# Kernel optimization log

Hardware: AMD Instinct MI355X
Metric: run time of the kernel (lower is better)

Reference implementation:

```python
import jax, jax.numpy as jnp
import numpy as np

N_NODES = 100000
N_EDGES = 1000000
D_IN = 64
D_HID = 64


def gcn_norm(edge_index, edge_weight, num_nodes):
    """PyG gcn_norm with add_self_loops=True, fill_value=1.0.
    Returns augmented (row, col, norm) including self loops."""
    loop = jnp.arange(num_nodes)
    row = jnp.concatenate([edge_index[0], loop])
    col = jnp.concatenate([edge_index[1], loop])
    ew = jnp.concatenate([edge_weight, jnp.ones((num_nodes,), edge_weight.dtype)])
    deg = jnp.zeros((num_nodes,), ew.dtype).at[col].add(ew)
    dinv = jnp.where(deg > 0, jax.lax.rsqrt(deg), 0.0).astype(ew.dtype)
    norm = dinv[row] * ew * dinv[col]  # [E + N]
    return row, col, norm


def gcn_conv(h, row, col, norm, W, b, num_nodes):
    """out[col] += norm * (h @ W)[row]; then add bias."""
    hw = h @ W  # [N, d_out] dense transform first (as PyG GCNConv)
    msg = norm[:, None] * hw[row]  # gather + scale  [E+N, d_out]
    out = jnp.zeros((num_nodes, W.shape[1]), h.dtype).at[col].add(msg)
    return out + b


def setup_inputs() -> dict:
    key = jax.random.key(0)
    ks = jax.random.split(key, 12)
    x = jax.random.normal(ks[0], (N_NODES, D_IN), jnp.float32)
    edge_index = jax.random.randint(ks[1], (2, N_EDGES), 0, N_NODES, jnp.int64)
    edge_weight = jax.random.uniform(ks[2], (N_EDGES,), jnp.float32)
    batch = jnp.zeros((N_NODES,), jnp.int64)

    def glorot(k, fan_in, fan_out):
        s = jnp.sqrt(6.0 / (fan_in + fan_out))
        return jax.random.uniform(k, (fan_in, fan_out), jnp.float32, -s, s)

    return {
        "x": x, "edge_index": edge_index, "edge_weight": edge_weight, "batch": batch,
        "W_in": glorot(ks[3], D_IN, D_HID), "b_in": jnp.zeros((D_HID,), jnp.float32),
        "W1": glorot(ks[4], D_HID, D_HID), "b1": jnp.zeros((D_HID,), jnp.float32),
        "W2": glorot(ks[5], D_HID, D_HID), "b2": jnp.zeros((D_HID,), jnp.float32),
        "Wf": glorot(ks[6], D_HID, 1), "bf": jnp.zeros((1,), jnp.float32),
    }


def reference(x, edge_index, edge_weight, batch, W_in, b_in, W1, b1, W2, b2, Wf, bf):
    n = x.shape[0]
    row, col, norm = gcn_norm(edge_index, edge_weight, n)  # shared across layers
    h = jax.nn.relu(gcn_conv(x, row, col, norm, W_in, b_in, n))
    h = jax.nn.relu(gcn_conv(h, row, col, norm, W1, b1, n) + h)
    h = jax.nn.relu(gcn_conv(h, row, col, norm, W2, b2, n) + h)
    out = gcn_conv(h, row, col, norm, Wf, bf, n)  # [N, 1]
    return out
```

## Files before the change

kernel.cpp:

```cpp
#include <hip/hip_runtime.h>

#define NN 100000
#define NE 1000000
#define D 64

using short8 = __attribute__((ext_vector_type(8))) short;
using f32x4  = __attribute__((ext_vector_type(4))) float;

__device__ __forceinline__ float bf2f(unsigned short u) {
    return __uint_as_float(((unsigned int)u) << 16);
}
__device__ __forceinline__ unsigned short f2bf(float f) {
    unsigned int u = __float_as_uint(f);
    u += 0x7fffu + ((u >> 16) & 1u);
    return (unsigned short)(u >> 16);
}

__global__ void count_pos_kernel(const int* __restrict__ col, int* __restrict__ cnt,
                                 int* __restrict__ epos, int E) {
    int e = blockIdx.x * blockDim.x + threadIdx.x;
    if (e < E) epos[e] = atomicAdd(&cnt[col[e]], 1);
}

__global__ void scanA(const int* __restrict__ cnt, int* __restrict__ rowptr,
                      int* __restrict__ bsum, int n) {
    __shared__ int s[256];
    int t = threadIdx.x;
    int i = blockIdx.x * 256 + t;
    int orig = (i < n) ? cnt[i] : 0;
    s[t] = orig;
    __syncthreads();
#pragma unroll
    for (int o = 1; o < 256; o <<= 1) {
        int v = (t >= o) ? s[t - o] : 0;
        __syncthreads();
        s[t] += v;
        __syncthreads();
    }
    if (i < n) rowptr[i] = s[t] - orig;
    if (t == 255) bsum[blockIdx.x] = s[t];
}

__global__ void scanB(int* __restrict__ bsum, int nb) {
    __shared__ int s[512];
    int t = threadIdx.x;
    int orig = (t < nb) ? bsum[t] : 0;
    s[t] = orig;
    __syncthreads();
#pragma unroll
    for (int o = 1; o < 512; o <<= 1) {
        int v = (t >= o) ? s[t - o] : 0;
        __syncthreads();
        s[t] += v;
        __syncthreads();
    }
    if (t < nb) bsum[t] = s[t] - orig;
}

__global__ void scanC(int* __restrict__ rowptr, const int* __restrict__ bsum, int n) {
    int i = blockIdx.x * 256 + threadIdx.x;
    if (i < n) rowptr[i] += bsum[i >> 8];
}

__global__ void place_kernel(const int* __restrict__ row, const int* __restrict__ col,
                             const float* __restrict__ ew, const int* __restrict__ epos,
                             const int* __restrict__ rowptr, int2* __restrict__ sedge, int E) {
    int e = blockIdx.x * blockDim.x + threadIdx.x;
    if (e < E) {
        int c = col[e];
        int p = rowptr[c] + epos[e];
        sedge[p] = make_int2(row[e], __float_as_int(ew[e]));
    }
}

__global__ void dinv_kernel(const int* __restrict__ rowptr, const int* __restrict__ cnt,
                            const int2* __restrict__ sedge, float* __restrict__ dinv, int n) {
    int i = blockIdx.x * blockDim.x + threadIdx.x;
    if (i >= n) return;
    int s = rowptr[i], d = cnt[i];
    float sum = 1.0f;
    for (int e = s; e < s + d; ++e) sum += __int_as_float(sedge[e].y);
    dinv[i] = rsqrtf(sum);
}

__global__ void wscale_kernel(const int* __restrict__ rowptr, const int* __restrict__ cnt,
                              int2* __restrict__ sedge, const float* __restrict__ dinv, int n) {
    int c = blockIdx.x * blockDim.x + threadIdx.x;
    if (c >= n) return;
    int s = rowptr[c], d = cnt[c];
    float dc = dinv[c];
    for (int e = s; e < s + d; ++e) {
        int2 ed = sedge[e];
        float w = __int_as_float(ed.y) * dinv[ed.x] * dc;
        sedge[e] = make_int2(ed.x, __float_as_int(w));
    }
}

__global__ void wtrans3(const float* __restrict__ W0, const float* __restrict__ W1,
                        const float* __restrict__ W2, unsigned short* __restrict__ T0,
                        unsigned short* __restrict__ T1, unsigned short* __restrict__ T2) {
    int b = blockIdx.x >> 4;
    int i = (blockIdx.x & 15) * 256 + threadIdx.x;
    const float* W = (b == 0) ? W0 : (b == 1) ? W1 : W2;
    unsigned short* T = (b == 0) ? T0 : (b == 1) ? T1 : T2;
    int k = i >> 6, j = i & 63;
    T[j * 64 + k] = f2bf(W[k * 64 + j]);
}

__global__ __launch_bounds__(256) void gemm_mfma(const float* __restrict__ H,
                                                 const unsigned short* __restrict__ Wt,
                                                 unsigned short* __restrict__ out16, int n) {
    int wave = threadIdx.x >> 6;
    int lane = threadIdx.x & 63;
    int r = lane & 15;
    int kg = lane >> 4;
    int base = blockIdx.x * 64 + wave * 16;
    int node = base + r;
    bool rv = node < n;
    const float* hrow = H + (size_t)(rv ? node : 0) * D;

    short8 a[2];
#pragma unroll
    for (int kk = 0; kk < 2; ++kk) {
        float4 f0, f1;
        if (rv) {
            f0 = *(const float4*)(hrow + kk * 32 + kg * 8);
            f1 = *(const float4*)(hrow + kk * 32 + kg * 8 + 4);
        } else {
            f0 = make_float4(0.f, 0.f, 0.f, 0.f);
            f1 = f0;
        }
        short8 v;
        v[0] = (short)f2bf(f0.x); v[1] = (short)f2bf(f0.y);
        v[2] = (short)f2bf(f0.z); v[3] = (short)f2bf(f0.w);
        v[4] = (short)f2bf(f1.x); v[5] = (short)f2bf(f1.y);
        v[6] = (short)f2bf(f1.z); v[7] = (short)f2bf(f1.w);
        a[kk] = v;
    }

    f32x4 acc[4];
#pragma unroll
    for (int jt = 0; jt < 4; ++jt) acc[jt] = (f32x4){0.f, 0.f, 0.f, 0.f};

#pragma unroll
    for (int jt = 0; jt < 4; ++jt) {
        short8 b0 = *(const short8*)(Wt + ((jt * 16 + r) * 64 + kg * 8));
        short8 b1 = *(const short8*)(Wt + ((jt * 16 + r) * 64 + 32 + kg * 8));
        acc[jt] = __builtin_amdgcn_mfma_f32_16x16x32_bf16(a[0], b0, acc[jt], 0, 0, 0);
        acc[jt] = __builtin_amdgcn_mfma_f32_16x16x32_bf16(a[1], b1, acc[jt], 0, 0, 0);
    }

#pragma unroll
    for (int i = 0; i < 4; ++i) {
        int orow = base + 4 * kg + i;
        if (orow < n) {
            unsigned short* o = out16 + (size_t)orow * D + r;
#pragma unroll
            for (int jt = 0; jt < 4; ++jt) o[jt * 16] = f2bf(acc[jt][i]);
        }
    }
}

__global__ void gather2_kernel(const int* __restrict__ rowptr, const int* __restrict__ cnt,
                               const int2* __restrict__ sedge,
                               const ushort2* __restrict__ hw16,
                               const float* __restrict__ dinv, const float* __restrict__ b,
                               const float* __restrict__ hres, float* __restrict__ hout, int n) {
    int c = blockIdx.x * 4 + (threadIdx.x >> 6);
    if (c >= n) return;
    int lane = threadIdx.x & 63;
    int half = lane >> 5;
    int fl = lane & 31;
    int start = rowptr[c];
    int deg = cnt[c];
    float ax = 0.0f, ay = 0.0f;
    for (int base = 0; base < deg; base += 64) {
        int rem = deg - base;
        int mm = rem < 64 ? rem : 64;
        int2 ed = make_int2(0, 0);
        if (base + lane < deg) ed = sedge[start + base + lane];
        int mr = (mm + 7) & ~7;
        for (int t = 0; t < mr; t += 8) {
            int rr[4]; int wb[4]; ushort2 u[4];
#pragma unroll
            for (int p = 0; p < 4; ++p) {
                int tt = t + 2 * p + half;
                rr[p] = __shfl(ed.x, tt, 64);
                wb[p] = __shfl(ed.y, tt, 64);
                u[p] = hw16[rr[p] * 32 + fl];
            }
#pragma unroll
            for (int p = 0; p < 4; ++p) {
                float w = __int_as_float(wb[p]);
                ax = fmaf(w, bf2f(u[p].x), ax);
                ay = fmaf(w, bf2f(u[p].y), ay);
            }
        }
    }
    ax += __shfl_xor(ax, 32, 64);
    ay += __shfl_xor(ay, 32, 64);
    if (half == 0) {
        float d = dinv[c];
        ushort2 su = hw16[c * 32 + fl];
        float2 bb = ((const float2*)b)[fl];
        float vx = ax + d * d * bf2f(su.x) + bb.x;
        float vy = ay + d * d * bf2f(su.y) + bb.y;
        if (hres) {
            float2 hr = ((const float2*)hres)[c * 32 + fl];
            vx += hr.x; vy += hr.y;
        }
        float2 o;
        o.x = fmaxf(vx, 0.0f);
        o.y = fmaxf(vy, 0.0f);
        ((float2*)hout)[c * 32 + fl] = o;
    }
}

__global__ void gemv_final(const float* __restrict__ H, const float* __restrict__ Wf,
                           float* __restrict__ hwf, int n) {
    int node = blockIdx.x * 4 + (threadIdx.x >> 6);
    if (node >= n) return;
    int k = threadIdx.x & 63;
    float v = H[node * D + k] * Wf[k];
#pragma unroll
    for (int off = 32; off > 0; off >>= 1) v += __shfl_down(v, off, 64);
    if (k == 0) hwf[node] = v;
}

__global__ void gather1_kernel(const int* __restrict__ rowptr, const int* __restrict__ cnt,
                               const int2* __restrict__ sedge, const float* __restrict__ hwf,
                               const float* __restrict__ dinv, const float* __restrict__ bf,
                               float* __restrict__ out, int n) {
    int c = blockIdx.x * blockDim.x + threadIdx.x;
    if (c >= n) return;
    int s = rowptr[c];
    int e1 = s + cnt[c];
    float acc = 0.0f;
    for (int e = s; e < e1; ++e) {
        int2 ed = sedge[e];
        acc = fmaf(__int_as_float(ed.y), hwf[ed.x], acc);
    }
    float d = dinv[c];
    out[c] = acc + d * d * hwf[c] + bf[0];
}

extern "C" void kernel_launch(void* const* d_in, const int* in_sizes, int n_in,
                              void* d_out, int out_size, void* d_ws, size_t ws_size,
                              hipStream_t stream) {
    const float* x    = (const float*)d_in[0];
    const int*   ei   = (const int*)d_in[1];
    const float* ew   = (const float*)d_in[2];
    const float* W_in = (const float*)d_in[4];
    const float* b_in = (const float*)d_in[5];
    const float* W1   = (const float*)d_in[6];
    const float* b1   = (const float*)d_in[7];
    const float* W2   = (const float*)d_in[8];
    const float* b2   = (const float*)d_in[9];
    const float* Wf   = (const float*)d_in[10];
    const float* bf   = (const float*)d_in[11];
    float* out = (float*)d_out;

    const int E = NE, n = NN;
    const int* row = ei;
    const int* col = ei + E;

    char* ws = (char*)d_ws;
    size_t off = 0;
    auto alloc = [&](size_t nbytes) {
        void* p = (void*)(ws + off);
        off += ((nbytes + 255) / 256) * 256;
        return p;
    };
    int*   cnt    = (int*)alloc((size_t)n * 4);
    int*   rowptr = (int*)alloc((size_t)n * 4);
    int*   epos   = (int*)alloc((size_t)E * 4);
    int*   bsum   = (int*)alloc(512 * 4);
    int2*  sedge  = (int2*)alloc((size_t)E * 8);
    float* dinv   = (float*)alloc((size_t)n * 4);
    unsigned short* hw16 = (unsigned short*)alloc((size_t)n * D * 2);
    float* hA     = (float*)alloc((size_t)n * D * 4);
    float* hB     = (float*)alloc((size_t)n * D * 4);
    float* hwf    = (float*)alloc((size_t)n * 4);
    unsigned short* Wt0 = (unsigned short*)alloc(D * D * 2);
    unsigned short* Wt1 = (unsigned short*)alloc(D * D * 2);
    unsigned short* Wt2 = (unsigned short*)alloc(D * D * 2);

    const int nbA = (n + 255) / 256;
    const int egrid = (E + 255) / 256;
    const int ngrid = (n + 255) / 256;
    const int mfma_grid = (n + 63) / 64;
    const int wave_grid = (n + 3) / 4;

    wtrans3<<<48, 256, 0, stream>>>(W_in, W1, W2, Wt0, Wt1, Wt2);

    hipMemsetAsync(cnt, 0, n * sizeof(int), stream);
    count_pos_kernel<<<egrid, 256, 0, stream>>>(col, cnt, epos, E);
    scanA<<<nbA, 256, 0, stream>>>(cnt, rowptr, bsum, n);
    scanB<<<1, 512, 0, stream>>>(bsum, nbA);
    scanC<<<nbA, 256, 0, stream>>>(rowptr, bsum, n);
    place_kernel<<<egrid, 256, 0, stream>>>(row, col, ew, epos, rowptr, sedge, E);
    dinv_kernel<<<ngrid, 256, 0, stream>>>(rowptr, cnt, sedge, dinv, n);
    wscale_kernel<<<ngrid, 256, 0, stream>>>(rowptr, cnt, sedge, dinv, n);

    gemm_mfma<<<mfma_grid, 256, 0, stream>>>(x, Wt0, hw16, n);
    gather2_kernel<<<wave_grid, 256, 0, stream>>>(rowptr, cnt, sedge, (const ushort2*)hw16,
                                                  dinv, b_in, nullptr, hA, n);

    gemm_mfma<<<mfma_grid, 256, 0, stream>>>(hA, Wt1, hw16, n);
    gather2_kernel<<<wave_grid, 256, 0, stream>>>(rowptr, cnt, sedge, (const ushort2*)hw16,
                                                  dinv, b1, hA, hB, n);

    gemm_mfma<<<mfma_grid, 256, 0, stream>>>(hB, Wt2, hw16, n);
    gather2_kernel<<<wave_grid, 256, 0, stream>>>(rowptr, cnt, sedge, (const ushort2*)hw16,
                                                  dinv, b2, hB, hA, n);

    gemv_final<<<wave_grid, 256, 0, stream>>>(hA, Wf, hwf, n);
    gather1_kernel<<<ngrid, 256, 0, stream>>>(rowptr, cnt, sedge, hwf, dinv, bf, out, n);
}
```

Before: 365.6 us.

## Widen gather to 8-byte loads and fuse final GEMV into last layer

The neighbor-gather kernel now has each lane load four bf16 features (ushort4) instead of two, so a wave processes four edges per step in 16-lane groups and reduces them with two cross-lane xor shuffles. The third layer's gather is fused with the final 64-to-1 projection, which removes the write and re-read of the hidden matrix and one kernel launch. The cost is more accumulator registers and an extra shuffle reduction stage.

```diff
diff --git a/kernel.cpp b/kernel.cpp
--- a/kernel.cpp
+++ b/kernel.cpp
@@ -161,70 +161,128 @@
     }
 }
 
-__global__ void gather2_kernel(const int* __restrict__ rowptr, const int* __restrict__ cnt,
+__global__ void gather4_kernel(const int* __restrict__ rowptr, const int* __restrict__ cnt,
                                const int2* __restrict__ sedge,
-                               const ushort2* __restrict__ hw16,
+                               const ushort4* __restrict__ hw16,
                                const float* __restrict__ dinv, const float* __restrict__ b,
                                const float* __restrict__ hres, float* __restrict__ hout, int n) {
     int c = blockIdx.x * 4 + (threadIdx.x >> 6);
     if (c >= n) return;
     int lane = threadIdx.x & 63;
-    int half = lane >> 5;
-    int fl = lane & 31;
+    int q = lane >> 4;
+    int fl = lane & 15;
     int start = rowptr[c];
     int deg = cnt[c];
-    float ax = 0.0f, ay = 0.0f;
+    float ax = 0.f, ay = 0.f, az = 0.f, aw = 0.f;
     for (int base = 0; base < deg; base += 64) {
         int rem = deg - base;
         int mm = rem < 64 ? rem : 64;
         int2 ed = make_int2(0, 0);
         if (base + lane < deg) ed = sedge[start + base + lane];
-        int mr = (mm + 7) & ~7;
-        for (int t = 0; t < mr; t += 8) {
-            int rr[4]; int wb[4]; ushort2 u[4];
+        int mr = (mm + 15) & ~15;
+        for (int t = 0; t < mr; t += 16) {
+            int rr[4]; int wb[4]; ushort4 u[4];
 #pragma unroll
             for (int p = 0; p < 4; ++p) {
-                int tt = t + 2 * p + half;
+                int tt = t + p * 4 + q;
                 rr[p] = __shfl(ed.x, tt, 64);
                 wb[p] = __shfl(ed.y, tt, 64);
-                u[p] = hw16[rr[p] * 32 + fl];
+                u[p] = hw16[rr[p] * 16 + fl];
             }
 #pragma unroll
             for (int p = 0; p < 4; ++p) {
                 float w = __int_as_float(wb[p]);
                 ax = fmaf(w, bf2f(u[p].x), ax);
                 ay = fmaf(w, bf2f(u[p].y), ay);
+                az = fmaf(w, bf2f(u[p].z), az);
+                aw = fmaf(w, bf2f(u[p].w), aw);
             }
         }
     }
-    ax += __shfl_xor(ax, 32, 64);
-    ay += __shfl_xor(ay, 32, 64);
-    if (half == 0) {
+    ax += __shfl_xor(ax, 16, 64); ay += __shfl_xor(ay, 16, 64);
+    az += __shfl_xor(az, 16, 64); aw += __shfl_xor(aw, 16, 64);
+    ax += __shfl_xor(ax, 32, 64); ay += __shfl_xor(ay, 32, 64);
+    az += __shfl_xor(az, 32, 64); aw += __shfl_xor(aw, 32, 64);
+    if (lane < 16) {
         float d = dinv[c];
-        ushort2 su = hw16[c * 32 + fl];
-        float2 bb = ((const float2*)b)[fl];
-        float vx = ax + d * d * bf2f(su.x) + bb.x;
-        float vy = ay + d * d * bf2f(su.y) + bb.y;
+        float dd = d * d;
+        ushort4 su = hw16[c * 16 + fl];
+        float4 bb = ((const float4*)b)[fl];
+        float vx = ax + dd * bf2f(su.x) + bb.x;
+        float vy = ay + dd * bf2f(su.y) + bb.y;
+        float vz = az + dd * bf2f(su.z) + bb.z;
+        float vw = aw + dd * bf2f(su.w) + bb.w;
         if (hres) {
-            float2 hr = ((const float2*)hres)[c * 32 + fl];
-            vx += hr.x; vy += hr.y;
-        }
-        float2 o;
-        o.x = fmaxf(vx, 0.0f);
-        o.y = fmaxf(vy, 0.0f);
-        ((float2*)hout)[c * 32 + fl] = o;
-    }
-}
-
-__global__ void gemv_final(const float* __restrict__ H, const float* __restrict__ Wf,
-                           float* __restrict__ hwf, int n) {
-    int node = blockIdx.x * 4 + (threadIdx.x >> 6);
-    if (node >= n) return;
-    int k = threadIdx.x & 63;
-    float v = H[node * D + k] * Wf[k];
-#pragma unroll
-    for (int off = 32; off > 0; off >>= 1) v += __shfl_down(v, off, 64);
-    if (k == 0) hwf[node] = v;
+            float4 hr = ((const float4*)hres)[c * 16 + fl];
+            vx += hr.x; vy += hr.y; vz += hr.z; vw += hr.w;
+        }
+        float4 o;
+        o.x = fmaxf(vx, 0.0f); o.y = fmaxf(vy, 0.0f);
+        o.z = fmaxf(vz, 0.0f); o.w = fmaxf(vw, 0.0f);
+        ((float4*)hout)[c * 16 + fl] = o;
+    }
+}
+
+__global__ void gather4_final_kernel(const int* __restrict__ rowptr, const int* __restrict__ cnt,
+                                     const int2* __restrict__ sedge,
+                                     const ushort4* __restrict__ hw16,
+                                     const float* __restrict__ dinv, const float* __restrict__ b,
+                                     const float* __restrict__ hres,
+                                     const float* __restrict__ Wf,
+                                     float* __restrict__ hwf, int n) {
+    int c = blockIdx.x * 4 + (threadIdx.x >> 6);
+    if (c >= n) return;
+    int lane = threadIdx.x & 63;
+    int q = lane >> 4;
+    int fl = lane & 15;
+    int start = rowptr[c];
+    int deg = cnt[c];
+    float ax = 0.f, ay = 0.f, az = 0.f, aw = 0.f;
+    for (int base = 0; base < deg; base += 64) {
+        int rem = deg - base;
+        int mm = rem < 64 ? rem : 64;
+        int2 ed = make_int2(0, 0);
+        if (base + lane < deg) ed = sedge[start + base + lane];
+        int mr = (mm + 15) & ~15;
+        for (int t = 0; t < mr; t += 16) {
+            int rr[4]; int wb[4]; ushort4 u[4];
+#pragma unroll
+            for (int p = 0; p < 4; ++p) {
+                int tt = t + p * 4 + q;
+                rr[p] = __shfl(ed.x, tt, 64);
+                wb[p] = __shfl(ed.y, tt, 64);
+                u[p] = hw16[rr[p] * 16 + fl];
+            }
+#pragma unroll
+            for (int p = 0; p < 4; ++p) {
+                float w = __int_as_float(wb[p]);
+                ax = fmaf(w, bf2f(u[p].x), ax);
+                ay = fmaf(w, bf2f(u[p].y), ay);
+                az = fmaf(w, bf2f(u[p].z), az);
+                aw = fmaf(w, bf2f(u[p].w), aw);
+            }
+        }
+    }
+    ax += __shfl_xor(ax, 16, 64); ay += __shfl_xor(ay, 16, 64);
+    az += __shfl_xor(az, 16, 64); aw += __shfl_xor(aw, 16, 64);
+    ax += __shfl_xor(ax, 32, 64); ay += __shfl_xor(ay, 32, 64);
+    az += __shfl_xor(az, 32, 64); aw += __shfl_xor(aw, 32, 64);
+    float d = dinv[c];
+    float dd = d * d;
+    ushort4 su = hw16[c * 16 + fl];
+    float4 bb = ((const float4*)b)[fl];
+    float4 hr = ((const float4*)hres)[c * 16 + fl];
+    float vx = fmaxf(ax + dd * bf2f(su.x) + bb.x + hr.x, 0.0f);
+    float vy = fmaxf(ay + dd * bf2f(su.y) + bb.y + hr.y, 0.0f);
+    float vz = fmaxf(az + dd * bf2f(su.z) + bb.z + hr.z, 0.0f);
+    float vw = fmaxf(aw + dd * bf2f(su.w) + bb.w + hr.w, 0.0f);
+    float4 wf = ((const float4*)Wf)[fl];
+    float part = vx * wf.x + vy * wf.y + vz * wf.z + vw * wf.w;
+    part += __shfl_xor(part, 8, 16);
+    part += __shfl_xor(part, 4, 16);
+    part += __shfl_xor(part, 2, 16);
+    part += __shfl_xor(part, 1, 16);
+    if (lane == 0) hwf[c] = part;
 }
 
 __global__ void gather1_kernel(const int* __restrict__ rowptr, const int* __restrict__ cnt,
@@ -303,17 +361,16 @@
     wscale_kernel<<<ngrid, 256, 0, stream>>>(rowptr, cnt, sedge, dinv, n);
 
     gemm_mfma<<<mfma_grid, 256, 0, stream>>>(x, Wt0, hw16, n);
-    gather2_kernel<<<wave_grid, 256, 0, stream>>>(rowptr, cnt, sedge, (const ushort2*)hw16,
+    gather4_kernel<<<wave_grid, 256, 0, stream>>>(rowptr, cnt, sedge, (const ushort4*)hw16,
                                                   dinv, b_in, nullptr, hA, n);
 
     gemm_mfma<<<mfma_grid, 256, 0, stream>>>(hA, Wt1, hw16, n);
-    gather2_kernel<<<wave_grid, 256, 0, stream>>>(rowptr, cnt, sedge, (const ushort2*)hw16,
+    gather4_kernel<<<wave_grid, 256, 0, stream>>>(rowptr, cnt, sedge, (const ushort4*)hw16,
                                                   dinv, b1, hA, hB, n);
 
     gemm_mfma<<<mfma_grid, 256, 0, stream>>>(hB, Wt2, hw16, n);
-    gather2_kernel<<<wave_grid, 256, 0, stream>>>(rowptr, cnt, sedge, (const ushort2*)hw16,
-                                                  dinv, b2, hB, hA, n);
-
-    gemv_final<<<wave_grid, 256, 0, stream>>>(hA, Wf, hwf, n);
+    gather4_final_kernel<<<wave_grid, 256, 0, stream>>>(rowptr, cnt, sedge, (const ushort4*)hw16,
+                                                        dinv, b2, hB, Wf, hwf, n);
+
     gather1_kernel<<<ngrid, 256, 0, stream>>>(rowptr, cnt, sedge, hwf, dinv, bf, out, n);
 }
```

Result: faster. 348.3 us (-4.7%).

## Split feature dimension into four quarter passes for cache-resident gathers, store activations in bf16

Applied to the files above, without the earlier changes.

The GEMM now writes its output as four column-quarter planes of 16 features each. Each quarter is gathered in a separate kernel pass, so the gathered table (about 3.2 MB) can stay in cache during the random-access aggregation. Hidden activations are stored in bf16 instead of fp32, and the final Wf dot product is fused into the last gather through atomics, which removes gemv_final. The cost is re-reading the edge list four times per layer, more kernel launches, and extra bf16 rounding of the residual activations.

```diff
diff --git a/kernel.cpp b/kernel.cpp
--- a/kernel.cpp
+++ b/kernel.cpp
@@ -107,9 +107,10 @@
     T[j * 64 + k] = f2bf(W[k * 64 + j]);
 }
 
-__global__ __launch_bounds__(256) void gemm_mfma(const float* __restrict__ H,
+template <int F32IN>
+__global__ __launch_bounds__(256) void gemm_mfma(const void* __restrict__ Hv,
                                                  const unsigned short* __restrict__ Wt,
-                                                 unsigned short* __restrict__ out16, int n) {
+                                                 unsigned short* __restrict__ qt, int n) {
     int wave = threadIdx.x >> 6;
     int lane = threadIdx.x & 63;
     int r = lane & 15;
@@ -117,25 +118,36 @@
     int base = blockIdx.x * 64 + wave * 16;
     int node = base + r;
     bool rv = node < n;
-    const float* hrow = H + (size_t)(rv ? node : 0) * D;
 
     short8 a[2];
-#pragma unroll
-    for (int kk = 0; kk < 2; ++kk) {
-        float4 f0, f1;
-        if (rv) {
-            f0 = *(const float4*)(hrow + kk * 32 + kg * 8);
-            f1 = *(const float4*)(hrow + kk * 32 + kg * 8 + 4);
-        } else {
-            f0 = make_float4(0.f, 0.f, 0.f, 0.f);
-            f1 = f0;
-        }
-        short8 v;
-        v[0] = (short)f2bf(f0.x); v[1] = (short)f2bf(f0.y);
-        v[2] = (short)f2bf(f0.z); v[3] = (short)f2bf(f0.w);
-        v[4] = (short)f2bf(f1.x); v[5] = (short)f2bf(f1.y);
-        v[6] = (short)f2bf(f1.z); v[7] = (short)f2bf(f1.w);
-        a[kk] = v;
+    if (F32IN) {
+        const float* hrow = (const float*)Hv + (size_t)(rv ? node : 0) * D;
+#pragma unroll
+        for (int kk = 0; kk < 2; ++kk) {
+            float4 f0, f1;
+            if (rv) {
+                f0 = *(const float4*)(hrow + kk * 32 + kg * 8);
+                f1 = *(const float4*)(hrow + kk * 32 + kg * 8 + 4);
+            } else {
+                f0 = make_float4(0.f, 0.f, 0.f, 0.f);
+                f1 = f0;
+            }
+            short8 v;
+            v[0] = (short)f2bf(f0.x); v[1] = (short)f2bf(f0.y);
+            v[2] = (short)f2bf(f0.z); v[3] = (short)f2bf(f0.w);
+            v[4] = (short)f2bf(f1.x); v[5] = (short)f2bf(f1.y);
+            v[6] = (short)f2bf(f1.z); v[7] = (short)f2bf(f1.w);
+            a[kk] = v;
+        }
+    } else {
+        const unsigned short* hrow = (const unsigned short*)Hv + (size_t)(rv ? node : 0) * D;
+#pragma unroll
+        for (int kk = 0; kk < 2; ++kk) {
+            short8 v;
+            if (rv) v = *(const short8*)(hrow + kk * 32 + kg * 8);
+            else    v = (short8){0, 0, 0, 0, 0, 0, 0, 0};
+            a[kk] = v;
+        }
     }
 
     f32x4 acc[4];
@@ -154,77 +166,144 @@
     for (int i = 0; i < 4; ++i) {
         int orow = base + 4 * kg + i;
         if (orow < n) {
-            unsigned short* o = out16 + (size_t)orow * D + r;
-#pragma unroll
-            for (int jt = 0; jt < 4; ++jt) o[jt * 16] = f2bf(acc[jt][i]);
-        }
-    }
-}
-
-__global__ void gather2_kernel(const int* __restrict__ rowptr, const int* __restrict__ cnt,
+#pragma unroll
+            for (int jt = 0; jt < 4; ++jt)
+                qt[(size_t)jt * n * 16 + (size_t)orow * 16 + r] = f2bf(acc[jt][i]);
+        }
+    }
+}
+
+template <int HAS_RES>
+__global__ void gatherq_kernel(const int* __restrict__ rowptr, const int* __restrict__ cnt,
                                const int2* __restrict__ sedge,
-                               const ushort2* __restrict__ hw16,
-                               const float* __restrict__ dinv, const float* __restrict__ b,
-                               const float* __restrict__ hres, float* __restrict__ hout, int n) {
+                               const unsigned short* __restrict__ qt,
+                               const float* __restrict__ dinv,
+                               const float* __restrict__ bq,
+                               const unsigned short* __restrict__ hres,
+                               unsigned short* __restrict__ hout,
+                               int p, int n) {
     int c = blockIdx.x * 4 + (threadIdx.x >> 6);
     if (c >= n) return;
     int lane = threadIdx.x & 63;
-    int half = lane >> 5;
-    int fl = lane & 31;
+    int eg = lane >> 2;
+    int fl4 = lane & 3;
     int start = rowptr[c];
     int deg = cnt[c];
-    float ax = 0.0f, ay = 0.0f;
+    float a0 = 0.f, a1 = 0.f, a2 = 0.f, a3 = 0.f;
     for (int base = 0; base < deg; base += 64) {
         int rem = deg - base;
         int mm = rem < 64 ? rem : 64;
-        int2 ed = make_int2(0, 0);
-        if (base + lane < deg) ed = sedge[start + base + lane];
-        int mr = (mm + 7) & ~7;
-        for (int t = 0; t < mr; t += 8) {
-            int rr[4]; int wb[4]; ushort2 u[4];
-#pragma unroll
-            for (int p = 0; p < 4; ++p) {
-                int tt = t + 2 * p + half;
-                rr[p] = __shfl(ed.x, tt, 64);
-                wb[p] = __shfl(ed.y, tt, 64);
-                u[p] = hw16[rr[p] * 32 + fl];
-            }
-#pragma unroll
-            for (int p = 0; p < 4; ++p) {
-                float w = __int_as_float(wb[p]);
-                ax = fmaf(w, bf2f(u[p].x), ax);
-                ay = fmaf(w, bf2f(u[p].y), ay);
-            }
-        }
-    }
-    ax += __shfl_xor(ax, 32, 64);
-    ay += __shfl_xor(ay, 32, 64);
-    if (half == 0) {
+        long long edb = 0;
+        if (base + lane < deg)
+            edb = __builtin_nontemporal_load((const long long*)(sedge + start + base + lane));
+        int edr = (int)(edb & 0xFFFFFFFFll);
+        int edw = (int)(edb >> 32);
+        int mr = (mm + 15) & ~15;
+        for (int t = 0; t < mr; t += 16) {
+            int tt = t + eg;
+            int rr = __shfl(edr, tt, 64);
+            float w = __int_as_float(__shfl(edw, tt, 64));
+            ushort4 u = *(const ushort4*)(qt + (size_t)rr * 16 + fl4 * 4);
+            a0 = fmaf(w, bf2f(u.x), a0);
+            a1 = fmaf(w, bf2f(u.y), a1);
+            a2 = fmaf(w, bf2f(u.z), a2);
+            a3 = fmaf(w, bf2f(u.w), a3);
+        }
+    }
+#pragma unroll
+    for (int off = 4; off <= 32; off <<= 1) {
+        a0 += __shfl_xor(a0, off, 64);
+        a1 += __shfl_xor(a1, off, 64);
+        a2 += __shfl_xor(a2, off, 64);
+        a3 += __shfl_xor(a3, off, 64);
+    }
+    if (lane < 4) {
         float d = dinv[c];
-        ushort2 su = hw16[c * 32 + fl];
-        float2 bb = ((const float2*)b)[fl];
-        float vx = ax + d * d * bf2f(su.x) + bb.x;
-        float vy = ay + d * d * bf2f(su.y) + bb.y;
-        if (hres) {
-            float2 hr = ((const float2*)hres)[c * 32 + fl];
-            vx += hr.x; vy += hr.y;
-        }
-        float2 o;
-        o.x = fmaxf(vx, 0.0f);
-        o.y = fmaxf(vy, 0.0f);
-        ((float2*)hout)[c * 32 + fl] = o;
-    }
-}
-
-__global__ void gemv_final(const float* __restrict__ H, const float* __restrict__ Wf,
-                           float* __restrict__ hwf, int n) {
-    int node = blockIdx.x * 4 + (threadIdx.x >> 6);
-    if (node >= n) return;
-    int k = threadIdx.x & 63;
-    float v = H[node * D + k] * Wf[k];
-#pragma unroll
-    for (int off = 32; off > 0; off >>= 1) v += __shfl_down(v, off, 64);
-    if (k == 0) hwf[node] = v;
+        float dd = d * d;
+        ushort4 su = *(const ushort4*)(qt + (size_t)c * 16 + fl4 * 4);
+        float4 bb = ((const float4*)bq)[fl4];
+        float v0 = a0 + dd * bf2f(su.x) + bb.x;
+        float v1 = a1 + dd * bf2f(su.y) + bb.y;
+        float v2 = a2 + dd * bf2f(su.z) + bb.z;
+        float v3 = a3 + dd * bf2f(su.w) + bb.w;
+        if (HAS_RES) {
+            unsigned long long hrb = __builtin_nontemporal_load(
+                (const unsigned long long*)(hres + (size_t)c * D + p * 16 + fl4 * 4));
+            v0 += bf2f((unsigned short)(hrb & 0xFFFF));
+            v1 += bf2f((unsigned short)((hrb >> 16) & 0xFFFF));
+            v2 += bf2f((unsigned short)((hrb >> 32) & 0xFFFF));
+            v3 += bf2f((unsigned short)((hrb >> 48) & 0xFFFF));
+        }
+        unsigned long long ob =
+            (unsigned long long)f2bf(fmaxf(v0, 0.f)) |
+            ((unsigned long long)f2bf(fmaxf(v1, 0.f)) << 16) |
+            ((unsigned long long)f2bf(fmaxf(v2, 0.f)) << 32) |
+            ((unsigned long long)f2bf(fmaxf(v3, 0.f)) << 48);
+        __builtin_nontemporal_store(ob,
+            (unsigned long long*)(hout + (size_t)c * D + p * 16 + fl4 * 4));
+    }
+}
+
+__global__ void gatherq_final_kernel(const int* __restrict__ rowptr, const int* __restrict__ cnt,
+                                     const int2* __restrict__ sedge,
+                                     const unsigned short* __restrict__ qt,
+                                     const float* __restrict__ dinv,
+                                     const float* __restrict__ bq,
+                                     const unsigned short* __restrict__ hres,
+                                     const float* __restrict__ Wfq,
+                                     float* __restrict__ hwf, int p, int n) {
+    int c = blockIdx.x * 4 + (threadIdx.x >> 6);
+    if (c >= n) return;
+    int lane = threadIdx.x & 63;
+    int eg = lane >> 2;
+    int fl4 = lane & 3;
+    int start = rowptr[c];
+    int deg = cnt[c];
+    float a0 = 0.f, a1 = 0.f, a2 = 0.f, a3 = 0.f;
+    for (int base = 0; base < deg; base += 64) {
+        int rem = deg - base;
+        int mm = rem < 64 ? rem : 64;
+        long long edb = 0;
+        if (base + lane < deg)
+            edb = __builtin_nontemporal_load((const long long*)(sedge + start + base + lane));
+        int edr = (int)(edb & 0xFFFFFFFFll);
+        int edw = (int)(edb >> 32);
+        int mr = (mm + 15) & ~15;
+        for (int t = 0; t < mr; t += 16) {
+            int tt = t + eg;
+            int rr = __shfl(edr, tt, 64);
+            float w = __int_as_float(__shfl(edw, tt, 64));
+            ushort4 u = *(const ushort4*)(qt + (size_t)rr * 16 + fl4 * 4);
+            a0 = fmaf(w, bf2f(u.x), a0);
+            a1 = fmaf(w, bf2f(u.y), a1);
+            a2 = fmaf(w, bf2f(u.z), a2);
+            a3 = fmaf(w, bf2f(u.w), a3);
+        }
+    }
+#pragma unroll
+    for (int off = 4; off <= 32; off <<= 1) {
+        a0 += __shfl_xor(a0, off, 64);
+        a1 += __shfl_xor(a1, off, 64);
+        a2 += __shfl_xor(a2, off, 64);
+        a3 += __shfl_xor(a3, off, 64);
+    }
+    if (lane < 4) {
+        float d = dinv[c];
+        float dd = d * d;
+        ushort4 su = *(const ushort4*)(qt + (size_t)c * 16 + fl4 * 4);
+        float4 bb = ((const float4*)bq)[fl4];
+        unsigned long long hrb = __builtin_nontemporal_load(
+            (const unsigned long long*)(hres + (size_t)c * D + p * 16 + fl4 * 4));
+        float v0 = fmaxf(a0 + dd * bf2f(su.x) + bb.x + bf2f((unsigned short)(hrb & 0xFFFF)), 0.f);
+        float v1 = fmaxf(a1 + dd * bf2f(su.y) + bb.y + bf2f((unsigned short)((hrb >> 16) & 0xFFFF)), 0.f);
+        float v2 = fmaxf(a2 + dd * bf2f(su.z) + bb.z + bf2f((unsigned short)((hrb >> 32) & 0xFFFF)), 0.f);
+        float v3 = fmaxf(a3 + dd * bf2f(su.w) + bb.w + bf2f((unsigned short)((hrb >> 48) & 0xFFFF)), 0.f);
+        float4 wf = ((const float4*)Wfq)[fl4];
+        float part = v0 * wf.x + v1 * wf.y + v2 * wf.z + v3 * wf.w;
+        part += __shfl_xor(part, 1, 64);
+        part += __shfl_xor(part, 2, 64);
+        if (lane == 0) atomicAdd(&hwf[c], part);
+    }
 }
 
 __global__ void gather1_kernel(const int* __restrict__ rowptr, const int* __restrict__ cnt,
@@ -237,8 +316,8 @@
     int e1 = s + cnt[c];
     float acc = 0.0f;
     for (int e = s; e < e1; ++e) {
-        int2 ed = sedge[e];
-        acc = fmaf(__int_as_float(ed.y), hwf[ed.x], acc);
+        long long edb = __builtin_nontemporal_load((const long long*)(sedge + e));
+        acc = fmaf(__int_as_float((int)(edb >> 32)), hwf[(int)(edb & 0xFFFFFFFFll)], acc);
     }
     float d = dinv[c];
     out[c] = acc + d * d * hwf[c] + bf[0];
@@ -278,8 +357,8 @@
     int2*  sedge  = (int2*)alloc((size_t)E * 8);
     float* dinv   = (float*)alloc((size_t)n * 4);
     unsigned short* hw16 = (unsigned short*)alloc((size_t)n * D * 2);
-    float* hA     = (float*)alloc((size_t)n * D * 4);
-    float* hB     = (float*)alloc((size_t)n * D * 4);
+    unsigned short* hA   = (unsigned short*)alloc((size_t)n * D * 2);
+    unsigned short* hB   = (unsigned short*)alloc((size_t)n * D * 2);
     float* hwf    = (float*)alloc((size_t)n * 4);
     unsigned short* Wt0 = (unsigned short*)alloc(D * D * 2);
     unsigned short* Wt1 = (unsigned short*)alloc(D * D * 2);
@@ -290,6 +369,7 @@
     const int ngrid = (n + 255) / 256;
     const int mfma_grid = (n + 63) / 64;
     const int wave_grid = (n + 3) / 4;
+    const size_t qstride = (size_t)n * 16;
 
     wtrans3<<<48, 256, 0, stream>>>(W_in, W1, W2, Wt0, Wt1, Wt2);
 
@@ -302,18 +382,21 @@
     dinv_kernel<<<ngrid, 256, 0, stream>>>(rowptr, cnt, sedge, dinv, n);
     wscale_kernel<<<ngrid, 256, 0, stream>>>(rowptr, cnt, sedge, dinv, n);
 
-    gemm_mfma<<<mfma_grid, 256, 0, stream>>>(x, Wt0, hw16, n);
-    gather2_kernel<<<wave_grid, 256, 0, stream>>>(rowptr, cnt, sedge, (const ushort2*)hw16,
-                                                  dinv, b_in, nullptr, hA, n);
-
-    gemm_mfma<<<mfma_grid, 256, 0, stream>>>(hA, Wt1, hw16, n);
-    gather2_kernel<<<wave_grid, 256, 0, stream>>>(rowptr, cnt, sedge, (const ushort2*)hw16,
-                                                  dinv, b1, hA, hB, n);
-
-    gemm_mfma<<<mfma_grid, 256, 0, stream>>>(hB, Wt2, hw16, n);
-    gather2_kernel<<<wave_grid, 256, 0, stream>>>(rowptr, cnt, sedge, (const ushort2*)hw16,
-                                                  dinv, b2, hB, hA, n);
-
-    gemv_final<<<wave_grid, 256, 0, stream>>>(hA, Wf, hwf, n);
+    gemm_mfma<1><<<mfma_grid, 256, 0, stream>>>(x, Wt0, hw16, n);
+    for (int p = 0; p < 4; ++p)
+        gatherq_kernel<0><<<wave_grid, 256, 0, stream>>>(rowptr, cnt, sedge,
+            hw16 + p * qstride, dinv, b_in + p * 16, nullptr, hA, p, n);
+
+    gemm_mfma<0><<<mfma_grid, 256, 0, stream>>>(hA, Wt1, hw16, n);
+    for (int p = 0; p < 4; ++p)
+        gatherq_kernel<1><<<wave_grid, 256, 0, stream>>>(rowptr, cnt, sedge,
+            hw16 + p * qstride, dinv, b1 + p * 16, hA, hB, p, n);
+
+    hipMemsetAsync(hwf, 0, n * sizeof(float), stream);
+    gemm_mfma<0><<<mfma_grid, 256, 0, stream>>>(hB, Wt2, hw16, n);
+    for (int p = 0; p < 4; ++p)
+        gatherq_final_kernel<<<wave_grid, 256, 0, stream>>>(rowptr, cnt, sedge,
+            hw16 + p * qstride, dinv, b2 + p * 16, hB, Wf + p * 16, hwf, p, n);
+
     gather1_kernel<<<ngrid, 256, 0, stream>>>(rowptr, cnt, sedge, hwf, dinv, bf, out, n);
 }
```

After: 728.0 us. 99.1% more time.
